# Kernel tuning notes

Measured on AMD Instinct MI355X. Metric: run time of the kernel, lower is better.

## Reference

```python
import jax, jax.numpy as jnp
import numpy as np

EPS = 1e-5  # torch GroupNorm default

def setup_inputs() -> dict:
    key = jax.random.key(0)
    k1, k2, k3, k4 = jax.random.split(key, 4)
    B = 1048576
    x = jax.random.uniform(k1, (B, 1, 1, 120), dtype=jnp.float32)  # [B,1,1,120]
    conv_w = jax.random.uniform(k2, (120, 1, 1, 120), dtype=jnp.float32, minval=-0.5, maxval=0.5)  # weight_org
    conv_b = jnp.zeros((120,), dtype=jnp.float32)
    gn_w = jnp.ones((120,), dtype=jnp.float32)
    gn_b = jnp.zeros((120,), dtype=jnp.float32)
    lin_w = jax.random.normal(k3, (1, 120), dtype=jnp.float32) * 0.1
    return {"x": x, "conv_w": conv_w, "conv_b": conv_b,
            "gn_w": gn_w, "gn_b": gn_b, "lin_w": lin_w}

def reference(x, conv_w, conv_b, gn_w, gn_b, lin_w):
    # Input binarize: sign(x - 0.5); weight binarize: sign(weight_org)
    xb = jnp.sign(x[:, 0, 0, :] - 0.5)        # [B,120], values in {-1,0,+1}
    wb = jnp.sign(conv_w[:, 0, 0, :])         # [120,120]
    # Conv2d with kernel (1,120) on [B,1,1,120] == GEMM; bias added after
    y = jnp.einsum('bk,ck->bc', xb, wb) + conv_b  # [B,120]
    # GroupNorm(1, 120): normalize over all 120 channels per sample
    mean = jnp.mean(y, axis=1, keepdims=True)
    var = jnp.var(y, axis=1, keepdims=True)
    y = (y - mean) * jax.lax.rsqrt(var + EPS) * gn_w + gn_b
    # Softsign
    y = y / (1.0 + jnp.abs(y))
    # BNNLinear forward: linear(input, weight) -- NO bias used
    out = y @ lin_w.T                          # [B,1]
    return out
```

## Files before the change

### kernel.cpp

```cpp
#include <hip/hip_runtime.h>

#define NCH 120

typedef int i32x4 __attribute__((ext_vector_type(4)));

__global__ void prep_kernel(const float* __restrict__ conv_w,
                            const float* __restrict__ conv_b,
                            const float* __restrict__ gn_w,
                            const float* __restrict__ gn_b,
                            const float* __restrict__ lin_w,
                            unsigned char* __restrict__ wsb)
{
    const int c = threadIdx.x;
    if (c >= 128) return;
    unsigned* row32 = (unsigned*)(wsb + c * 128);
    if (c < NCH) {
        for (int kw = 0; kw < 32; ++kw) {
            unsigned pk = 0u;
            for (int b = 0; b < 4; ++b) {
                const int k = kw * 4 + b;
                unsigned v = 0u;
                if (k < NCH) {
                    const float w = conv_w[c * NCH + k];
                    v = (w > 0.0f) ? 0x01u : ((w < 0.0f) ? 0xFFu : 0x00u);
                }
                pk |= v << (8 * b);
            }
            row32[kw] = pk;
        }
    } else {
        for (int kw = 0; kw < 32; ++kw) row32[kw] = 0u;
    }
    __syncthreads();

    {
        int s = 0;
        if (c < NCH)
            for (int r = 0; r < NCH; ++r)
                s += (int)(signed char)wsb[r * 128 + c];
        wsb[120 * 128 + c] = (unsigned char)((unsigned)s & 0xFFu);
    }

    float4 o;
    o.x = (c < NCH) ? conv_b[c] : 0.0f;
    o.y = (c < NCH) ? gn_w[c]   : 1.0f;
    o.z = (c < NCH) ? gn_b[c]   : 0.0f;
    o.w = (c < NCH) ? lin_w[c]  : 0.0f;
    ((float4*)(wsb + 16384))[c] = o;
}

__device__ __forceinline__ unsigned cvt4(float4 v) {
    unsigned b0 = (v.x > 0.5f) ? 0x01u : ((v.x < 0.5f) ? 0xFFu : 0x00u);
    unsigned b1 = (v.y > 0.5f) ? 0x01u : ((v.y < 0.5f) ? 0xFFu : 0x00u);
    unsigned b2 = (v.z > 0.5f) ? 0x01u : ((v.z < 0.5f) ? 0xFFu : 0x00u);
    unsigned b3 = (v.w > 0.5f) ? 0x01u : ((v.w < 0.5f) ? 0xFFu : 0x00u);
    return b0 | (b1 << 8) | (b2 << 16) | (b3 << 24);
}

__global__ __launch_bounds__(256) void bnn_kernel(
    const float* __restrict__ x,
    const unsigned char* __restrict__ wsb,
    float* __restrict__ out,
    int B, int num_tiles, int tiles_per_block)
{
    __shared__ float4 s_cf[128];

    const int tid  = threadIdx.x;
    const int lane = tid & 63;
    const int wv   = tid >> 6;
    const int l15  = lane & 15;
    const int lg   = lane >> 4;
    const bool padlane = (lg == 3);

    if (tid < 128) s_cf[tid] = ((const float4*)(wsb + 16384))[tid];
    __syncthreads();

    long bfrag[8][4];
#pragma unroll
    for (int t = 0; t < 8; ++t)
#pragma unroll
        for (int kc = 0; kc < 4; ++kc)
            bfrag[t][kc] = *(const long*)(wsb + (t * 16 + l15) * 128 + kc * 32 + lg * 8);

    float4 pf[8];
    {
        long long srow = (long long)blockIdx.x * 64 + wv * 16 + l15;
        if (srow > (long long)B - 1) srow = (long long)B - 1;
        const float* __restrict__ xr = x + srow * NCH;
#pragma unroll
        for (int j = 0; j < 8; ++j) {
            int off = (j >> 1) * 32 + lg * 8 + (j & 1) * 4;
            if (j >= 6 && padlane) off = (j & 1) * 4;
            pf[j] = *(const float4*)(xr + off);
        }
    }

    for (int it = 0; it < tiles_per_block; ++it) {
        const int tile = blockIdx.x + it * gridDim.x;
        if (tile >= num_tiles) break;
        const long long s0 = (long long)tile * 64 + wv * 16;

        long afrag[4];
#pragma unroll
        for (int kc = 0; kc < 4; ++kc) {
            unsigned w0 = cvt4(pf[kc * 2]);
            unsigned w1 = cvt4(pf[kc * 2 + 1]);
            if (kc == 3 && padlane) { w0 = 0u; w1 = 0u; }
            afrag[kc] = (long)(((unsigned long long)w1 << 32) | w0);
        }

        if (it + 1 < tiles_per_block) {
            int nt = blockIdx.x + (it + 1) * gridDim.x;
            if (nt > num_tiles - 1) nt = num_tiles - 1;
            long long srow = (long long)nt * 64 + wv * 16 + l15;
            if (srow > (long long)B - 1) srow = (long long)B - 1;
            const float* __restrict__ xr = x + srow * NCH;
#pragma unroll
            for (int j = 0; j < 8; ++j) {
                int off = (j >> 1) * 32 + lg * 8 + (j & 1) * 4;
                if (j >= 6 && padlane) off = (j & 1) * 4;
                pf[j] = *(const float4*)(xr + off);
            }
        }

        i32x4 acc[8];
#pragma unroll
        for (int t = 0; t < 8; ++t) acc[t] = (i32x4){0, 0, 0, 0};
#pragma unroll
        for (int kc = 0; kc < 4; ++kc)
#pragma unroll
            for (int t = 0; t < 8; ++t)
                acc[t] = __builtin_amdgcn_mfma_i32_16x16x32_i8(
                    afrag[kc], bfrag[t][kc], acc[t], 0, 0, 0);

        int S2[4] = {0, 0, 0, 0};
#pragma unroll
        for (int t = 0; t < 8; ++t)
#pragma unroll
            for (int q = 0; q < 4; ++q) {
                int y = acc[t][q];
                if (t == 7) y = (l15 == 8) ? 0 : y;
                S2[q] += y * y;
            }
#pragma unroll
        for (int m = 1; m <= 8; m <<= 1)
#pragma unroll
            for (int q = 0; q < 4; ++q)
                S2[q] += __shfl_xor(S2[q], m, 64);

        float rstd[4], nb[4];
#pragma unroll
        for (int q = 0; q < 4; ++q) {
            const int s1 = __shfl(acc[7][q], (lane & 48) | 8, 64);
            const float mean = (float)s1 * (1.0f / 120.0f);
            const float var  = (float)S2[q] * (1.0f / 120.0f) - mean * mean;
            rstd[q] = __builtin_amdgcn_rsqf(var + 1e-5f);
            nb[q]   = -mean * rstd[q];
        }

        float d[4] = {0.0f, 0.0f, 0.0f, 0.0f};
#pragma unroll
        for (int t = 0; t < 8; ++t) {
            const float4 cf = s_cf[t * 16 + l15];
#pragma unroll
            for (int q = 0; q < 4; ++q) {
                const float yf = (float)acc[t][q] + cf.x;
                const float n  = fmaf(yf, rstd[q], nb[q]);
                const float g  = fmaf(n, cf.y, cf.z);
                const float s  = g * __builtin_amdgcn_rcpf(1.0f + fabsf(g));
                d[q] = fmaf(s, cf.w, d[q]);
            }
        }
#pragma unroll
        for (int m = 1; m <= 8; m <<= 1)
#pragma unroll
            for (int q = 0; q < 4; ++q)
                d[q] += __shfl_xor(d[q], m, 64);

        if (l15 == 0) {
#pragma unroll
            for (int q = 0; q < 4; ++q) {
                const long long o = s0 + lg * 4 + q;
                if (o < (long long)B) out[o] = d[q];
            }
        }
    }
}

extern "C" void kernel_launch(void* const* d_in, const int* in_sizes, int n_in,
                              void* d_out, int out_size, void* d_ws, size_t ws_size,
                              hipStream_t stream) {
    const float* x      = (const float*)d_in[0];
    const float* conv_w = (const float*)d_in[1];
    const float* conv_b = (const float*)d_in[2];
    const float* gn_w   = (const float*)d_in[3];
    const float* gn_b   = (const float*)d_in[4];
    const float* lin_w  = (const float*)d_in[5];
    unsigned char* wsb = (unsigned char*)d_ws;
    float* out = (float*)d_out;

    const int B = in_sizes[0] / NCH;
    prep_kernel<<<1, 128, 0, stream>>>(conv_w, conv_b, gn_w, gn_b, lin_w, wsb);

    const int num_tiles = (B + 63) / 64;
    const int grid = num_tiles < 2048 ? num_tiles : 2048;
    const int tiles_per_block = (num_tiles + grid - 1) / grid;
    bnn_kernel<<<grid, 256, 0, stream>>>(x, wsb, out, B, num_tiles, tiles_per_block);
}
```

Before: 143.4 us.

## Stage binarized input through LDS with coalesced block-wide loads

Global loads of x switch from a per-row scattered pattern, where each lane reads float4 pieces of its own row, to contiguous block-wide float4 loads across the whole 64-row tile. Each load is binarized to int8 and written into a double-buffered LDS tile, and the MFMA A fragments are then read from LDS. The goal is fully coalesced streaming of the memory-bound input and avoiding re-reads of the padded lanes. The cost is an LDS round trip and a __syncthreads per tile.

```diff
diff --git a/kernel.cpp b/kernel.cpp
--- a/kernel.cpp
+++ b/kernel.cpp
@@ -63,6 +63,7 @@
     float* __restrict__ out,
     int B, int num_tiles, int tiles_per_block)
 {
+    __shared__ __align__(16) unsigned char s_xb[2][7680];
     __shared__ float4 s_cf[128];
 
     const int tid  = threadIdx.x;
@@ -73,7 +74,6 @@
     const bool padlane = (lg == 3);
 
     if (tid < 128) s_cf[tid] = ((const float4*)(wsb + 16384))[tid];
-    __syncthreads();
 
     long bfrag[8][4];
 #pragma unroll
@@ -82,46 +82,55 @@
         for (int kc = 0; kc < 4; ++kc)
             bfrag[t][kc] = *(const long*)(wsb + (t * 16 + l15) * 128 + kc * 32 + lg * 8);
 
-    float4 pf[8];
+    const long long maxf4 = (long long)B * 30 - 1;
+
+    unsigned sx[8];
     {
-        long long srow = (long long)blockIdx.x * 64 + wv * 16 + l15;
-        if (srow > (long long)B - 1) srow = (long long)B - 1;
-        const float* __restrict__ xr = x + srow * NCH;
-#pragma unroll
-        for (int j = 0; j < 8; ++j) {
-            int off = (j >> 1) * 32 + lg * 8 + (j & 1) * 4;
-            if (j >= 6 && padlane) off = (j & 1) * 4;
-            pf[j] = *(const float4*)(xr + off);
-        }
-    }
-
+        const long long t0 = (long long)blockIdx.x * 1920;
+#pragma unroll
+        for (int r = 0; r < 8; ++r) {
+            if (r < 7 || tid < 128) {
+                long long f4 = t0 + r * 256 + tid;
+                if (f4 > maxf4) f4 = maxf4;
+                sx[r] = cvt4(*(const float4*)(x + f4 * 4));
+            }
+        }
+    }
+
+    int cur = 0;
     for (int it = 0; it < tiles_per_block; ++it) {
         const int tile = blockIdx.x + it * gridDim.x;
         if (tile >= num_tiles) break;
         const long long s0 = (long long)tile * 64 + wv * 16;
 
+        unsigned* dst = (unsigned*)s_xb[cur];
+#pragma unroll
+        for (int r = 0; r < 8; ++r)
+            if (r < 7 || tid < 128) dst[r * 256 + tid] = sx[r];
+
+        float4 fr[8];
+        const int nt = blockIdx.x + (it + 1) * gridDim.x;
+        const bool havenext = (it + 1 < tiles_per_block) && (nt < num_tiles);
+        if (havenext) {
+            const long long tb = (long long)nt * 1920;
+#pragma unroll
+            for (int r = 0; r < 8; ++r) {
+                if (r < 7 || tid < 128) {
+                    long long f4 = tb + r * 256 + tid;
+                    if (f4 > maxf4) f4 = maxf4;
+                    fr[r] = *(const float4*)(x + f4 * 4);
+                }
+            }
+        }
+
+        __syncthreads();
+
+        const unsigned char* rowp = s_xb[cur] + (wv * 16 + l15) * 120 + lg * 8;
         long afrag[4];
 #pragma unroll
-        for (int kc = 0; kc < 4; ++kc) {
-            unsigned w0 = cvt4(pf[kc * 2]);
-            unsigned w1 = cvt4(pf[kc * 2 + 1]);
-            if (kc == 3 && padlane) { w0 = 0u; w1 = 0u; }
-            afrag[kc] = (long)(((unsigned long long)w1 << 32) | w0);
-        }
-
-        if (it + 1 < tiles_per_block) {
-            int nt = blockIdx.x + (it + 1) * gridDim.x;
-            if (nt > num_tiles - 1) nt = num_tiles - 1;
-            long long srow = (long long)nt * 64 + wv * 16 + l15;
-            if (srow > (long long)B - 1) srow = (long long)B - 1;
-            const float* __restrict__ xr = x + srow * NCH;
-#pragma unroll
-            for (int j = 0; j < 8; ++j) {
-                int off = (j >> 1) * 32 + lg * 8 + (j & 1) * 4;
-                if (j >= 6 && padlane) off = (j & 1) * 4;
-                pf[j] = *(const float4*)(xr + off);
-            }
-        }
+        for (int kc = 0; kc < 4; ++kc)
+            afrag[kc] = *(const long*)(rowp + kc * 32);
+        if (padlane) afrag[3] = 0;
 
         i32x4 acc[8];
 #pragma unroll
@@ -184,6 +193,13 @@
                 if (o < (long long)B) out[o] = d[q];
             }
         }
+
+        if (havenext) {
+#pragma unroll
+            for (int r = 0; r < 8; ++r)
+                if (r < 7 || tid < 128) sx[r] = cvt4(fr[r]);
+        }
+        cur ^= 1;
     }
 }
 
```

After: 147.0 us. 2.5% more time.

## Stage input tiles via async global-to-LDS loads with double buffering

Applied to the files above, without the earlier changes.

Replaces the per-lane register prefetch of strided float4 row pieces with fully coalesced contiguous 16-byte global_load_lds copies into a per-wave double-buffered LDS region. The next tile is staged while the current one is read from LDS, converted to int8 and fed to the MFMA, with explicit vmcnt waits. The goal is better coalescing and deeper overlap of HBM reads on this bandwidth-bound kernel. In exchange it uses about 61KB of LDS per block, which can lower occupancy, and it depends on hand-written waitcnt values being correct.

```diff
diff --git a/kernel.cpp b/kernel.cpp
--- a/kernel.cpp
+++ b/kernel.cpp
@@ -3,6 +3,8 @@
 #define NCH 120
 
 typedef int i32x4 __attribute__((ext_vector_type(4)));
+typedef const __attribute__((address_space(1))) void* gas_t;
+typedef __attribute__((address_space(3))) void* las_t;
 
 __global__ void prep_kernel(const float* __restrict__ conv_w,
                             const float* __restrict__ conv_b,
@@ -63,6 +65,7 @@
     float* __restrict__ out,
     int B, int num_tiles, int tiles_per_block)
 {
+    __shared__ float4 s_raw4[2][1920];
     __shared__ float4 s_cf[128];
 
     const int tid  = threadIdx.x;
@@ -73,7 +76,6 @@
     const bool padlane = (lg == 3);
 
     if (tid < 128) s_cf[tid] = ((const float4*)(wsb + 16384))[tid];
-    __syncthreads();
 
     long bfrag[8][4];
 #pragma unroll
@@ -82,44 +84,57 @@
         for (int kc = 0; kc < 4; ++kc)
             bfrag[t][kc] = *(const long*)(wsb + (t * 16 + l15) * 128 + kc * 32 + lg * 8);
 
-    float4 pf[8];
-    {
-        long long srow = (long long)blockIdx.x * 64 + wv * 16 + l15;
-        if (srow > (long long)B - 1) srow = (long long)B - 1;
-        const float* __restrict__ xr = x + srow * NCH;
-#pragma unroll
-        for (int j = 0; j < 8; ++j) {
-            int off = (j >> 1) * 32 + lg * 8 + (j & 1) * 4;
-            if (j >= 6 && padlane) off = (j & 1) * 4;
-            pf[j] = *(const float4*)(xr + off);
-        }
-    }
-
+    __syncthreads();
+
+    const char* xb = (const char*)x;
+    char* lb = (char*)&s_raw4[0][0];
+    const unsigned maxbyte = (unsigned)B * 480u - 16u;
+
+    auto STAGE = [&](int buf, int t) {
+        const unsigned gb = (unsigned)t * 30720u + (unsigned)wv * 7680u
+                          + (unsigned)lane * 16u;
+        const unsigned lbase = (unsigned)buf * 30720u + (unsigned)wv * 7680u;
+#pragma unroll
+        for (int r = 0; r < 7; ++r) {
+            unsigned g = gb + (unsigned)r * 1024u;
+            if (g > maxbyte) g = maxbyte;
+            __builtin_amdgcn_global_load_lds((gas_t)(xb + g),
+                                             (las_t)(lb + lbase + r * 1024u),
+                                             16, 0, 0);
+        }
+        if (lane < 32) {
+            unsigned g = gb + 7168u;
+            if (g > maxbyte) g = maxbyte;
+            __builtin_amdgcn_global_load_lds((gas_t)(xb + g),
+                                             (las_t)(lb + lbase + 7168u),
+                                             16, 0, 0);
+        }
+    };
+
+    if (blockIdx.x < (unsigned)num_tiles) STAGE(0, blockIdx.x);
+
+    int cur = 0;
     for (int it = 0; it < tiles_per_block; ++it) {
         const int tile = blockIdx.x + it * gridDim.x;
         if (tile >= num_tiles) break;
         const long long s0 = (long long)tile * 64 + wv * 16;
 
+        const int nt = blockIdx.x + (it + 1) * gridDim.x;
+        const bool have = (it + 1 < tiles_per_block) && (nt < num_tiles);
+        if (have) STAGE(cur ^ 1, nt);
+
+        if (have) asm volatile("s_waitcnt vmcnt(8)" ::: "memory");
+        else      asm volatile("s_waitcnt vmcnt(0)" ::: "memory");
+
+        const float4* rp = &s_raw4[cur][0] + (wv * 16 + l15) * 30 + lg * 2;
         long afrag[4];
 #pragma unroll
         for (int kc = 0; kc < 4; ++kc) {
-            unsigned w0 = cvt4(pf[kc * 2]);
-            unsigned w1 = cvt4(pf[kc * 2 + 1]);
-            if (kc == 3 && padlane) { w0 = 0u; w1 = 0u; }
-            afrag[kc] = (long)(((unsigned long long)w1 << 32) | w0);
-        }
-
-        if (it + 1 < tiles_per_block) {
-            int nt = blockIdx.x + (it + 1) * gridDim.x;
-            if (nt > num_tiles - 1) nt = num_tiles - 1;
-            long long srow = (long long)nt * 64 + wv * 16 + l15;
-            if (srow > (long long)B - 1) srow = (long long)B - 1;
-            const float* __restrict__ xr = x + srow * NCH;
-#pragma unroll
-            for (int j = 0; j < 8; ++j) {
-                int off = (j >> 1) * 32 + lg * 8 + (j & 1) * 4;
-                if (j >= 6 && padlane) off = (j & 1) * 4;
-                pf[j] = *(const float4*)(xr + off);
+            if (kc == 3 && padlane) { afrag[3] = 0; }
+            else {
+                float4 f0 = rp[kc * 8];
+                float4 f1 = rp[kc * 8 + 1];
+                afrag[kc] = (long)(((unsigned long long)cvt4(f1) << 32) | cvt4(f0));
             }
         }
 
@@ -184,6 +199,8 @@
                 if (o < (long long)B) out[o] = d[q];
             }
         }
+
+        cur ^= 1;
     }
 }
 
```

Measured after the change: 152.6 us. 6.4% more time.
